# Kernel optimization log

Hardware: AMD Instinct MI355X
Metric: run time of the kernel (lower is better)

Reference implementation:

```python
import jax, jax.numpy as jnp
import numpy as np

BUCKET_SIZE = 64
N_HASHES = 8


def setup_inputs() -> dict:
    key = jax.random.key(0)
    ks = jax.random.split(key, 8)
    B, S, D = 4, 4096, 512
    n_buckets = S // BUCKET_SIZE  # 64
    x = jax.random.normal(ks[0], (B, S, D), dtype=jnp.float32)
    rotations = jax.random.normal(ks[1], (1, D, N_HASHES, n_buckets // 2), dtype=jnp.float32)
    w_qk = jax.random.normal(ks[2], (D, D), dtype=jnp.float32) * 0.02
    b_qk = jax.random.normal(ks[3], (D,), dtype=jnp.float32) * 0.02
    w_v = jax.random.normal(ks[4], (D, D), dtype=jnp.float32) * 0.02
    b_v = jax.random.normal(ks[5], (D,), dtype=jnp.float32) * 0.02
    w_out = jax.random.normal(ks[6], (D, D), dtype=jnp.float32) * 0.02
    b_out = jax.random.normal(ks[7], (D,), dtype=jnp.float32) * 0.02
    return {"x": x, "rotations": rotations, "w_qk": w_qk, "b_qk": b_qk,
            "w_v": w_v, "b_v": b_v, "w_out": w_out, "b_out": b_out}


def reference(x, rotations, w_qk, b_qk, w_v, b_v, w_out, b_out):
    B, S, D = x.shape
    T = S  # seqlen is already a multiple of 2*bucket_size -> no padding
    n_buckets = T // BUCKET_SIZE
    qk = x @ w_qk + b_qk            # [B, T, D]
    v = x @ w_v + b_v               # [B, T, D]

    # --- LSH bucketing ---
    rot = jnp.einsum('btf,fhi->bhti', qk, rotations[0])      # [B, H, T, nb/2]
    rot = jnp.concatenate([rot, -rot], axis=-1)              # [B, H, T, nb]
    buckets = jnp.argmax(rot, axis=-1)                       # [B, H, T]
    offsets = (jnp.arange(N_HASHES) * n_buckets)[None, :, None]
    buckets = (buckets + offsets).reshape(B, -1)             # [B, H*T]

    # --- stable sort by (bucket, position) ---
    ticker = jnp.arange(N_HASHES * T)[None, :]
    buckets_and_t = T * buckets + ticker % T                 # unique keys
    sticker = jnp.argsort(buckets_and_t, axis=-1)            # sorted ticker values
    undo_sort = jnp.argsort(sticker, axis=-1)
    st = sticker % T                                         # token positions

    # --- gather Q/K/V into sorted order ---
    idx = jnp.broadcast_to(st[:, :, None], (B, N_HASHES * T, D))
    sqk = jnp.take_along_axis(qk, idx, axis=1)               # [B, H*T, D]
    sv = jnp.take_along_axis(v, idx, axis=1)

    # --- chunked attention (no softmax, as in the original module) ---
    chunks = N_HASHES * n_buckets
    bq = sqk.reshape(B, chunks, BUCKET_SIZE, D)
    bv = sv.reshape(B, chunks, BUCKET_SIZE, D)
    norm = jnp.maximum(jnp.linalg.norm(bq, axis=-1, keepdims=True), 1e-12)
    bk = bq / norm                                           # F.normalize(p=2)
    dots = jnp.einsum('buie,buje->buij', bq, bk) * (D ** -0.5)
    bo = jnp.einsum('buij,buje->buie', dots, bv)             # [B, chunks, bs, D]

    # --- scatter back and combine hash rounds ---
    so = bo.reshape(B, -1, D)
    uidx = jnp.broadcast_to(undo_sort[:, :, None], (B, N_HASHES * T, D))
    o = jnp.take_along_axis(so, uidx, axis=1)
    out = o.reshape(B, N_HASHES, T, D).sum(axis=1)           # sum over hash rounds
    return out @ w_out + b_out
```

## Files before the change

### kernel.cpp

```cpp
#include <hip/hip_runtime.h>


typedef __attribute__((ext_vector_type(8))) short short8;
typedef __attribute__((ext_vector_type(4))) float f32x4;
typedef unsigned short ushort_t;

__device__ __forceinline__ ushort_t f2b(float f) {
  union { float f; unsigned u; } x; x.f = f;
  unsigned r = x.u + 0x7fffu + ((x.u >> 16) & 1u);
  return (ushort_t)(r >> 16);
}
__device__ __forceinline__ float b2f(unsigned b) {
  union { unsigned u; float f; } x; x.u = b << 16;
  return x.f;
}
__device__ __forceinline__ void gload16(void* lds, const void* gp) {
  __builtin_amdgcn_global_load_lds(
      (const __attribute__((address_space(1))) unsigned int*)gp,
      (__attribute__((address_space(3))) unsigned int*)lds, 16, 0, 0);
}

__global__ __launch_bounds__(256) void prep_kernel(
    const float* __restrict__ x, const float* __restrict__ w_qk,
    const float* __restrict__ b_qk, const float* __restrict__ R,
    const float* __restrict__ w_v, const float* __restrict__ w_out,
    ushort_t* __restrict__ xh, ushort_t* __restrict__ xl,
    ushort_t* __restrict__ wqkT, ushort_t* __restrict__ wvT, ushort_t* __restrict__ woT,
    ushort_t* __restrict__ W2Th, ushort_t* __restrict__ W2Tl, float* __restrict__ b2,
    int* __restrict__ mcount)
{
  __shared__ float t[32][33];
  __shared__ float wrow[512];
  const int blk = blockIdx.x, tid = threadIdx.x;
  if (blk == 0 && tid == 0) mcount[0] = 0;

  if (blk < 4096) {
    const int i = blk * 256 + tid;
    const float4 a = *(const float4*)(x + (size_t)i * 8);
    const float4 c = *(const float4*)(x + (size_t)i * 8 + 4);
    float v[8] = { a.x, a.y, a.z, a.w, c.x, c.y, c.z, c.w };
    ushort_t hi[8], lo[8];
    #pragma unroll
    for (int k = 0; k < 8; ++k) {
      hi[k] = f2b(v[k]);
      lo[k] = f2b(v[k] - b2f(hi[k]));
    }
    *(uint4*)(xh + (size_t)i * 8) = *(const uint4*)hi;
    *(uint4*)(xl + (size_t)i * 8) = *(const uint4*)lo;
  } else if (blk < 4864) {
    const int idx = blk - 4096;
    const int mat = idx >> 8, r = idx & 255;
    const float* W  = (mat == 0) ? w_qk : (mat == 1) ? w_v : w_out;
    ushort_t*   Wt  = (mat == 0) ? wqkT : (mat == 1) ? wvT : woT;
    const int bx = (r & 15) * 32, by = (r >> 4) * 32;
    const int tx = tid & 31, ty = tid >> 5;
    #pragma unroll
    for (int j = 0; j < 4; ++j)
      t[ty + j*8][tx] = W[(size_t)(by + ty + j*8) * 512 + bx + tx];
    __syncthreads();
    #pragma unroll
    for (int j = 0; j < 4; ++j)
      Wt[(size_t)(bx + ty + j*8) * 512 + by + tx] = f2b(t[tx][ty + j*8]);
  } else {
    const int e = blk - 4864, j = tid;
    const float* src = (e < 512) ? (w_qk + (size_t)e * 512) : b_qk;
    wrow[j]       = src[j];
    wrow[j + 256] = src[j + 256];
    __syncthreads();
    float acc = 0.f;
    for (int f = 0; f < 512; ++f)
      acc = fmaf(wrow[f], R[(size_t)f * 256 + j], acc);
    if (e < 512) {
      const ushort_t hi = f2b(acc);
      W2Th[(size_t)j * 512 + e] = hi;
      W2Tl[(size_t)j * 512 + e] = f2b(acc - b2f(hi));
    } else {
      b2[j] = acc;
    }
  }
}

__global__ __launch_bounds__(256, 2) void gemm_mfma(
    const ushort_t* __restrict__ A, const ushort_t* __restrict__ Wt,
    const float* __restrict__ bias, float* __restrict__ Cf,
    ushort_t* __restrict__ Cb, int out_bf16)
{
  __shared__ __align__(16) char Al[32768];
  __shared__ __align__(16) char Bl[32768];
  const int bm = blockIdx.x * 128, bn = blockIdx.y * 128;
  const int tid = threadIdx.x, w = tid >> 6, l = tid & 63;
  const int m = l & 15, gq = l >> 4;
  f32x4 acc[2][8] = {};

#define STAGE1(NB, K0) { \
    _Pragma("unroll") \
    for (int j = 0; j < 4; ++j) { \
      const int row = w * 32 + j * 8 + (l >> 3); \
      const int ch = (l & 7) ^ (row & 7); \
      const int dst = (NB) * 16384 + w * 4096 + j * 1024 + l * 16; \
      gload16(Al + dst, A  + (size_t)(bm + row) * 512 + (K0) + ch * 8); \
      gload16(Bl + dst, Wt + (size_t)(bn + row) * 512 + (K0) + ch * 8); \
    } }

  STAGE1(0, 0)
  __syncthreads();
  for (int t = 0; t < 8; ++t) {
    const int cur = t & 1;
    if (t < 7) STAGE1(cur ^ 1, (t + 1) * 64)
    #pragma unroll
    for (int ks = 0; ks < 2; ++ks) {
      short8 bfr[8];
      #pragma unroll
      for (int tj = 0; tj < 8; ++tj) {
        const int brow = tj * 16 + m;
        bfr[tj] = *(const short8*)(Bl + cur * 16384 + ((brow * 128 + ks * 64 + gq * 16) ^ ((brow & 7) << 4)));
      }
      #pragma unroll
      for (int ti = 0; ti < 2; ++ti) {
        const int arow = w * 32 + ti * 16 + m;
        const short8 af = *(const short8*)(Al + cur * 16384 + ((arow * 128 + ks * 64 + gq * 16) ^ ((arow & 7) << 4)));
        #pragma unroll
        for (int tj = 0; tj < 8; ++tj)
          acc[ti][tj] = __builtin_amdgcn_mfma_f32_16x16x32_bf16(af, bfr[tj], acc[ti][tj], 0, 0, 0);
      }
    }
    __syncthreads();
  }
#undef STAGE1
  #pragma unroll
  for (int ti = 0; ti < 2; ++ti)
    #pragma unroll
    for (int tj = 0; tj < 8; ++tj) {
      const int col = bn + tj * 16 + m;
      const float bvv = bias[col];
      #pragma unroll
      for (int r2 = 0; r2 < 4; ++r2) {
        const int row = bm + w * 32 + ti * 16 + gq * 4 + r2;
        const float oo = acc[ti][tj][r2] + bvv;
        if (out_bf16) Cb[(size_t)row * 512 + col] = f2b(oo);
        else          Cf[(size_t)row * 512 + col] = oo;
      }
    }
}

__global__ __launch_bounds__(256, 3) void gemm_mfma_x2(
    const ushort_t* __restrict__ Ah, const ushort_t* __restrict__ Al,
    const ushort_t* __restrict__ Wt, const float* __restrict__ bias,
    ushort_t* __restrict__ Cb)
{
  __shared__ __align__(16) char AH[16384], AL[16384], BH[16384];
  const int bm = blockIdx.x * 128, bn = blockIdx.y * 128;
  const int tid = threadIdx.x, w = tid >> 6, l = tid & 63;
  const int m = l & 15, gq = l >> 4;
  f32x4 acc[2][8] = {};
  for (int k0 = 0; k0 < 512; k0 += 64) {
    #pragma unroll
    for (int j = 0; j < 4; ++j) {
      const int row = w * 32 + j * 8 + (l >> 3);
      const int ch = (l & 7) ^ (row & 7);
      const int dst = w * 4096 + j * 1024 + l * 16;
      gload16(AH + dst, Ah + (size_t)(bm + row) * 512 + k0 + ch * 8);
      gload16(AL + dst, Al + (size_t)(bm + row) * 512 + k0 + ch * 8);
      gload16(BH + dst, Wt + (size_t)(bn + row) * 512 + k0 + ch * 8);
    }
    __syncthreads();
    #pragma unroll
    for (int ks = 0; ks < 2; ++ks) {
      short8 bfr[8];
      #pragma unroll
      for (int tj = 0; tj < 8; ++tj) {
        const int brow = tj * 16 + m;
        bfr[tj] = *(const short8*)(BH + ((brow * 128 + ks * 64 + gq * 16) ^ ((brow & 7) << 4)));
      }
      #pragma unroll
      for (int ti = 0; ti < 2; ++ti) {
        const int arow = w * 32 + ti * 16 + m;
        const int aa = (arow * 128 + ks * 64 + gq * 16) ^ ((arow & 7) << 4);
        const short8 ah8 = *(const short8*)(AH + aa);
        const short8 al8 = *(const short8*)(AL + aa);
        #pragma unroll
        for (int tj = 0; tj < 8; ++tj) {
          acc[ti][tj] = __builtin_amdgcn_mfma_f32_16x16x32_bf16(ah8, bfr[tj], acc[ti][tj], 0, 0, 0);
          acc[ti][tj] = __builtin_amdgcn_mfma_f32_16x16x32_bf16(al8, bfr[tj], acc[ti][tj], 0, 0, 0);
        }
      }
    }
    __syncthreads();
  }
  #pragma unroll
  for (int ti = 0; ti < 2; ++ti)
    #pragma unroll
    for (int tj = 0; tj < 8; ++tj) {
      const int col = bn + tj * 16 + m;
      const float bvv = bias[col];
      #pragma unroll
      for (int r2 = 0; r2 < 4; ++r2) {
        const int row = bm + w * 32 + ti * 16 + gq * 4 + r2;
        Cb[(size_t)row * 512 + col] = f2b(acc[ti][tj][r2] + bvv);
      }
    }
}

__global__ __launch_bounds__(256, 2) void rot3_mfma(
    const ushort_t* __restrict__ Ah, const ushort_t* __restrict__ Al,
    const ushort_t* __restrict__ Bh, const ushort_t* __restrict__ Bl,
    const float* __restrict__ b2, float* __restrict__ rot)
{
  __shared__ __align__(16) char AH[16384], AL[16384], BH[16384], BL[16384];
  const int bm = blockIdx.x * 128, bn = blockIdx.y * 128;
  const int tid = threadIdx.x, w = tid >> 6, l = tid & 63;
  const int m = l & 15, gq = l >> 4;
  f32x4 acc[2][8] = {};
  for (int k0 = 0; k0 < 512; k0 += 64) {
    #pragma unroll
    for (int j = 0; j < 4; ++j) {
      const int row = w * 32 + j * 8 + (l >> 3);
      const int ch = (l & 7) ^ (row & 7);
      const int dst = w * 4096 + j * 1024 + l * 16;
      gload16(AH + dst, Ah + (size_t)(bm + row) * 512 + k0 + ch * 8);
      gload16(AL + dst, Al + (size_t)(bm + row) * 512 + k0 + ch * 8);
      gload16(BH + dst, Bh + (size_t)(bn + row) * 512 + k0 + ch * 8);
      gload16(BL + dst, Bl + (size_t)(bn + row) * 512 + k0 + ch * 8);
    }
    __syncthreads();
    #pragma unroll
    for (int ks = 0; ks < 2; ++ks) {
      short8 bh8[8], bl8[8];
      #pragma unroll
      for (int tj = 0; tj < 8; ++tj) {
        const int ba = ((tj * 16 + m) * 128 + ks * 64 + gq * 16) ^ (((tj * 16 + m) & 7) << 4);
        bh8[tj] = *(const short8*)(BH + ba);
        bl8[tj] = *(const short8*)(BL + ba);
      }
      #pragma unroll
      for (int ti = 0; ti < 2; ++ti) {
        const int arow = w * 32 + ti * 16 + m;
        const int aa = (arow * 128 + ks * 64 + gq * 16) ^ ((arow & 7) << 4);
        const short8 ah8 = *(const short8*)(AH + aa);
        const short8 al8 = *(const short8*)(AL + aa);
        #pragma unroll
        for (int tj = 0; tj < 8; ++tj) {
          acc[ti][tj] = __builtin_amdgcn_mfma_f32_16x16x32_bf16(ah8, bh8[tj], acc[ti][tj], 0, 0, 0);
          acc[ti][tj] = __builtin_amdgcn_mfma_f32_16x16x32_bf16(al8, bh8[tj], acc[ti][tj], 0, 0, 0);
          acc[ti][tj] = __builtin_amdgcn_mfma_f32_16x16x32_bf16(ah8, bl8[tj], acc[ti][tj], 0, 0, 0);
        }
      }
    }
    __syncthreads();
  }
  #pragma unroll
  for (int ti = 0; ti < 2; ++ti)
    #pragma unroll
    for (int tj = 0; tj < 8; ++tj) {
      const int col = bn + tj * 16 + m;
      const float bvv = b2[col];
      #pragma unroll
      for (int r2 = 0; r2 < 4; ++r2) {
        const int row = bm + w * 32 + ti * 16 + gq * 4 + r2;
        rot[(size_t)row * 256 + col] = acc[ti][tj][r2] + bvv;
      }
    }
}

__global__ __launch_bounds__(256) void argmax_scale(
    const float* __restrict__ rot, int* __restrict__ buckets,
    int* __restrict__ mlist, int* __restrict__ mcount, float tau,
    const ushort_t* __restrict__ qh, float* __restrict__ scale)
{
  const int blk = blockIdx.x;
  if (blk < 16384) {
    const int tok = blk;
    const int j = threadIdx.x;
    const float r = rot[(size_t)tok * 256 + j];
    float m1, m2; int i1;
    if (r >= 0.f) { m1 = r;  i1 = j & 31;        m2 = -r; }
    else          { m1 = -r; i1 = (j & 31) + 32; m2 = r;  }
    #pragma unroll
    for (int off = 16; off; off >>= 1) {
      const float om1 = __shfl_xor(m1, off);
      const int   oi1 = __shfl_xor(i1, off);
      const float om2 = __shfl_xor(m2, off);
      float loser;
      if (om1 > m1 || (om1 == m1 && oi1 < i1)) { loser = m1; m1 = om1; i1 = oi1; }
      else loser = om1;
      m2 = fmaxf(fmaxf(m2, om2), loser);
    }
    if ((j & 31) == 0) {
      const int h = j >> 5, b = tok >> 12, t = tok & 4095;
      buckets[((b << 3) + h) * 4096 + t] = i1;
      if (m1 - m2 < tau) {
        const int k = atomicAdd(mcount, 1);
        mlist[k] = (((b << 3) + h) << 12) | t;
      }
    }
  } else {
    const int wave = threadIdx.x >> 6, lane = threadIdx.x & 63;
    const int tok = (blk - 16384) * 4 + wave;
    const uint4 H = *(const uint4*)(qh + (size_t)tok * 512 + lane * 8);
    const unsigned* hp = (const unsigned*)&H;
    float s = 0.f;
    #pragma unroll
    for (int e = 0; e < 4; ++e) {
      const float v0 = b2f(hp[e] & 0xffffu);
      const float v1 = b2f(hp[e] >> 16);
      s += v0 * v0 + v1 * v1;
    }
    #pragma unroll
    for (int off = 32; off; off >>= 1) s += __shfl_down(s, off);
    if (lane == 0) {
      const float nn = fmaxf(sqrtf(s), 1e-12f);
      scale[tok] = 0.044194173824159216f / nn;
    }
  }
}

__global__ __launch_bounds__(512) void bucket_fallback(
    const float* __restrict__ x, const float* __restrict__ w_qk,
    const float* __restrict__ b_qk, const float* __restrict__ R,
    const int* __restrict__ mlist, const int* __restrict__ mcount,
    int* __restrict__ buckets)
{
  __shared__ float qkrow[512];
  const int n = mcount[0];
  for (int ii = blockIdx.x; ii < n; ii += gridDim.x) {
    const int mm = mlist[ii];
    const int bh = mm >> 12, t = mm & 4095;
    const int b = bh >> 3, h = bh & 7;
    const float* xr = x + ((size_t)b * 4096 + t) * 512;
    {
      const int c = threadIdx.x;
      float a0 = 0.f;
      for (int f = 0; f < 512; ++f) a0 = fmaf(xr[f], w_qk[(size_t)f * 512 + c], a0);
      qkrow[c] = a0 + b_qk[c];
    }
    __syncthreads();
    if (threadIdx.x < 32) {
      const int col = h * 32 + threadIdx.x;
      float a0 = 0.f;
      for (int f = 0; f < 512; ++f) a0 = fmaf(qkrow[f], R[(size_t)f * 256 + col], a0);
      float m1; int i1;
      if (a0 >= 0.f) { m1 = a0;  i1 = threadIdx.x; }
      else           { m1 = -a0; i1 = threadIdx.x + 32; }
      #pragma unroll
      for (int off = 16; off; off >>= 1) {
        const float om = __shfl_xor(m1, off);
        const int   oi = __shfl_xor(i1, off);
        if (om > m1 || (om == m1 && oi < i1)) { m1 = om; i1 = oi; }
      }
      if (threadIdx.x == 0) buckets[(size_t)bh * 4096 + t] = i1;
    }
    __syncthreads();
  }
}

__global__ __launch_bounds__(256) void sort_kernel(
    const int* __restrict__ buckets, int* __restrict__ st)
{
  __shared__ int bk_lds[4096];
  __shared__ int cnt[64][64];
  __shared__ int bstart[64];
  const int tid = threadIdx.x;
  const int base = blockIdx.x * 4096;
  const int wave = tid >> 6, lane = tid & 63;
  const unsigned long long lt = (1ull << lane) - 1ull;

  for (int t = tid; t < 4096; t += 256) bk_lds[t] = buckets[base + t];
  for (int i = tid; i < 4096; i += 256) ((int*)cnt)[i] = 0;
  __syncthreads();

  for (int c = wave; c < 64; c += 4) {
    const int bk = bk_lds[c * 64 + lane];
    unsigned long long mask = ~0ull;
    #pragma unroll
    for (int bit = 0; bit < 6; ++bit) {
      const unsigned long long bb = __ballot((bk >> bit) & 1);
      mask &= ((bk >> bit) & 1) ? bb : ~bb;
    }
    if ((mask & lt) == 0)
      cnt[c][bk] = __popcll(mask);
  }
  __syncthreads();

  if (tid < 64) {
    int run = 0;
    for (int c = 0; c < 64; ++c) {
      const int v = cnt[c][tid];
      cnt[c][tid] = run;
      run += v;
    }
    int ex = run;
    #pragma unroll
    for (int off = 1; off < 64; off <<= 1) {
      const int nn = __shfl_up(ex, off);
      if (lane >= off) ex += nn;
    }
    bstart[tid] = ex - run;
  }
  __syncthreads();

  for (int c = wave; c < 64; c += 4) {
    const int tok = c * 64 + lane;
    const int bk = bk_lds[tok];
    unsigned long long mask = ~0ull;
    #pragma unroll
    for (int bit = 0; bit < 6; ++bit) {
      const unsigned long long bb = __ballot((bk >> bit) & 1);
      mask &= ((bk >> bit) & 1) ? bb : ~bb;
    }
    const int rank = (int)__popcll(mask & lt);
    st[base + bstart[bk] + cnt[c][bk] + rank] = tok;
  }
}

__global__ __launch_bounds__(256, 2) void attn_mfma(
    const ushort_t* __restrict__ qk_b, const ushort_t* __restrict__ v_b,
    const float* __restrict__ scale, const int* __restrict__ st,
    ushort_t* __restrict__ so, int g, int hbase)
{
  __shared__ __align__(16) char Q[32768];
  __shared__ __align__(16) char VT[32768];
  __shared__ __align__(16) char P[8192];
  __shared__ int   stt[64];
  __shared__ float scl[64];

  const int blk = blockIdx.x;
  const int cpg = g * 64;
  const int b = blk / cpg, rem = blk % cpg;
  const int hl = rem >> 6, c = rem & 63;
  const int tid = threadIdx.x, w = tid >> 6, l = tid & 63;
  const int m = l & 15, gq = l >> 4;
  const int srow = tid >> 5, su = tid & 31;

  if (tid < 64) {
    const int s = st[(size_t)((b * 8 + hbase + hl) * 4096) + c * 64 + tid];
    stt[tid] = s;
    scl[tid] = scale[b * 4096 + s];
  }
  __syncthreads();

  const size_t qkbase = (size_t)b * 4096;
  uint4 rg[8];

#define LOADG(SRC, HALF) { \
    _Pragma("unroll") \
    for (int it = 0; it < 8; ++it) { \
      const int row = it * 8 + srow; \
      rg[it] = *(const uint4*)((SRC) + (qkbase + stt[row]) * 512 + (HALF) * 256 + su * 8); \
    } }
#define WRITEQ() { \
    _Pragma("unroll") \
    for (int it = 0; it < 8; ++it) { \
      const int row = it * 8 + srow; \
      *(uint4*)(Q + ((row * 512 + su * 16) ^ ((row & 7) << 4))) = rg[it]; \
    } }
#define WRITEVT() { \
    _Pragma("unroll") \
    for (int it = 0; it < 8; ++it) { \
      const int j = it * 8 + srow; \
      const ushort_t* e = (const ushort_t*)&rg[it]; \
      _Pragma("unroll") \
      for (int ee = 0; ee < 8; ++ee) { \
        const int d = su * 8 + ee; \
        *(ushort_t*)(VT + ((d * 128 + j * 2) ^ (((d ^ (d >> 3)) & 7) << 4))) = e[ee]; \
      } \
    } }
#define COMPUTE_S() { \
    _Pragma("unroll") \
    for (int kf = 0; kf < 8; ++kf) { \
      const int arow = w * 16 + m; \
      const short8 af = *(const short8*)(Q + ((arow * 512 + kf * 64 + gq * 16) ^ ((arow & 7) << 4))); \
      _Pragma("unroll") \
      for (int jt = 0; jt < 4; ++jt) { \
        const int brow = jt * 16 + m; \
        const short8 bf = *(const short8*)(Q + ((brow * 512 + kf * 64 + gq * 16) ^ ((brow & 7) << 4))); \
        accS[jt] = __builtin_amdgcn_mfma_f32_16x16x32_bf16(af, bf, accS[jt], 0, 0, 0); \
      } \
    } }
#define COMPUTE_PV(ACCO) { \
    _Pragma("unroll") \
    for (int dt = 0; dt < 16; ++dt) { \
      _Pragma("unroll") \
      for (int kf = 0; kf < 2; ++kf) { \
        const int d = dt * 16 + m; \
        const short8 bv = *(const short8*)(VT + ((d * 128 + kf * 64 + gq * 16) ^ (((d ^ (d >> 3)) & 7) << 4))); \
        ACCO[dt] = __builtin_amdgcn_mfma_f32_16x16x32_bf16(ap[kf], bv, ACCO[dt], 0, 0, 0); \
      } \
    } }
#define BOUNCE(ACCO) { \
    _Pragma("unroll") \
    for (int dt = 0; dt < 16; ++dt) \
      _Pragma("unroll") \
      for (int r = 0; r < 4; ++r) { \
        const int i = w * 16 + gq * 4 + r; \
        const int dcol = dt * 16 + m; \
        *(ushort_t*)(Q + ((i * 512 + dcol * 2) ^ ((i & 7) << 4))) = f2b(ACCO[dt][r]); \
      } }
#define FLUSH(HALF) { \
    _Pragma("unroll") \
    for (int it = 0; it < 8; ++it) { \
      const int row = it * 8 + srow; \
      const uint4 dat = *(const uint4*)(Q + ((row * 512 + su * 16) ^ ((row & 7) << 4))); \
      *(uint4*)(so + (sobase + stt[row]) * 512 + (HALF) * 256 + su * 8) = dat; \
    } }

  f32x4 accS[4] = {};

  LOADG(qk_b, 0)
  WRITEQ()
  __syncthreads();
  LOADG(qk_b, 1)
  COMPUTE_S()
  __syncthreads();
  WRITEQ()
  __syncthreads();
  LOADG(v_b, 0)
  COMPUTE_S()
  __syncthreads();

  #pragma unroll
  for (int jt = 0; jt < 4; ++jt)
    #pragma unroll
    for (int r = 0; r < 4; ++r) {
      const int i = w * 16 + gq * 4 + r;
      const int j = jt * 16 + m;
      *(ushort_t*)(P + ((i * 128 + j * 2) ^ ((i & 7) << 4))) = f2b(accS[jt][r] * scl[j]);
    }
  WRITEVT()
  __syncthreads();

  const size_t sobase = (size_t)(b * g + hl) * 4096;
  LOADG(v_b, 1)
  short8 ap[2];
  #pragma unroll
  for (int kf = 0; kf < 2; ++kf) {
    const int i = w * 16 + m;
    ap[kf] = *(const short8*)(P + ((i * 128 + kf * 64 + gq * 16) ^ ((i & 7) << 4)));
  }
  f32x4 accO[16] = {};
  COMPUTE_PV(accO)
  __syncthreads();

  WRITEVT()
  BOUNCE(accO)
  __syncthreads();

  FLUSH(0)
  f32x4 accO2[16] = {};
  COMPUTE_PV(accO2)
  __syncthreads();

  BOUNCE(accO2)
  __syncthreads();
  FLUSH(1)

#undef LOADG
#undef WRITEQ
#undef WRITEVT
#undef COMPUTE_S
#undef COMPUTE_PV
#undef BOUNCE
#undef FLUSH
}

__global__ __launch_bounds__(256) void gather_kernel(
    const ushort_t* __restrict__ so, ushort_t* __restrict__ o_b, int g, int first)
{
  const int tok = blockIdx.x;
  const int b = tok >> 12, t = tok & 4095;
  const int d0 = threadIdx.x * 2;
  ushort_t* dst = o_b + (size_t)tok * 512 + d0;
  float ax = 0.f, ay = 0.f;
  if (!first) {
    const unsigned u = *(const unsigned*)dst;
    ax = b2f(u & 0xffffu); ay = b2f(u >> 16);
  }
  const size_t stride = (size_t)4096 * 512;
  const ushort_t* src = so + ((size_t)(b * g) * 4096 + t) * 512 + d0;
  for (int hlp = 0; hlp < g; ++hlp) {
    const unsigned u = *(const unsigned*)src;
    ax += b2f(u & 0xffffu);
    ay += b2f(u >> 16);
    src += stride;
  }
  *(unsigned*)dst = ((unsigned)f2b(ay) << 16) | (unsigned)f2b(ax);
}

extern "C" void kernel_launch(void* const* d_in, const int* in_sizes, int n_in,
                              void* d_out, int out_size, void* d_ws, size_t ws_size,
                              hipStream_t stream) {
  const float* x         = (const float*)d_in[0];
  const float* rotations = (const float*)d_in[1];
  const float* w_qk      = (const float*)d_in[2];
  const float* b_qk      = (const float*)d_in[3];
  const float* w_v       = (const float*)d_in[4];
  const float* b_v       = (const float*)d_in[5];
  const float* w_out     = (const float*)d_in[6];
  const float* b_out     = (const float*)d_in[7];
  float* out = (float*)d_out;
  char* ws = (char*)d_ws;

  ushort_t* xh      = (ushort_t*)(ws);
  ushort_t* xl      = (ushort_t*)(ws + 16777216);
  ushort_t* qk_hi   = (ushort_t*)(ws + 33554432);
  ushort_t* v_b     = (ushort_t*)(ws + 50331648);
  float*    rot     = (float*)(ws + 67108864);
  ushort_t* o_b     = (ushort_t*)(ws + 67108864);
  ushort_t* wqkTh   = (ushort_t*)(ws + 83886080);
  ushort_t* wvT     = (ushort_t*)(ws + 84410368);
  ushort_t* woT     = (ushort_t*)(ws + 84934656);
  ushort_t* W2Th    = (ushort_t*)(ws + 85458944);
  ushort_t* W2Tl    = (ushort_t*)(ws + 85721088);
  float*    b2      = (float*)(ws + 85983232);
  float*    scale   = (float*)(ws + 85987328);
  int*      buckets = (int*)(ws + 86052864);
  int*      st      = (int*)(ws + 86577152);
  int*      mlist   = (int*)(ws + 87101440);
  int*      mcount  = (int*)(ws + 87625728);
  ushort_t* so      = (ushort_t*)(ws + 87629824);
  const size_t so_off = 87629824;

  int g = 1;
  for (int cand = 8; cand >= 1; cand >>= 1)
    if (so_off + (size_t)cand * 16777216ull <= ws_size) { g = cand; break; }

  const dim3 blk256(256);
  hipLaunchKernelGGL(prep_kernel, dim3(5377), blk256, 0, stream,
                     x, w_qk, b_qk, rotations, w_v, w_out,
                     xh, xl, wqkTh, wvT, woT, W2Th, W2Tl, b2, mcount);

  hipLaunchKernelGGL(gemm_mfma_x2, dim3(128, 4), blk256, 0, stream, xh, xl, wqkTh, b_qk, qk_hi);
  hipLaunchKernelGGL(gemm_mfma, dim3(128, 4), blk256, 0, stream, xh, wvT, b_v, (float*)0, v_b, 1);
  hipLaunchKernelGGL(rot3_mfma, dim3(128, 2), blk256, 0, stream, xh, xl, W2Th, W2Tl, b2, rot);

  hipLaunchKernelGGL(argmax_scale, dim3(20480), blk256, 0, stream,
                     rot, buckets, mlist, mcount, 1.5e-3f, qk_hi, scale);
  hipLaunchKernelGGL(bucket_fallback, dim3(1024), dim3(512), 0, stream,
                     x, w_qk, b_qk, rotations, mlist, mcount, buckets);
  hipLaunchKernelGGL(sort_kernel, dim3(32), blk256, 0, stream, buckets, st);

  const int passes = 8 / g;
  for (int p = 0; p < passes; ++p) {
    const int hbase = p * g;
    hipLaunchKernelGGL(attn_mfma, dim3(4 * g * 64), blk256, 0, stream,
                       qk_hi, v_b, scale, st, so, g, hbase);
    hipLaunchKernelGGL(gather_kernel, dim3(16384), blk256, 0, stream,
                       so, o_b, g, (p == 0) ? 1 : 0);
  }

  hipLaunchKernelGGL(gemm_mfma, dim3(128, 4), blk256, 0, stream, o_b, woT, b_out, out, (ushort_t*)0, 0);
}
```

Before: 256.5 us.

## Fuse QK and V projections into one GEMM with interleaved QKV output

Replaces the separate hi/lo split-precision QK GEMM and the V GEMM with a single launch. Each token's QK and V rows are written side by side in one buffer with a 1024-wide row stride. The QK projection drops the low-part correction pass and now uses only xh, halving its MFMA work at some cost in QK precision. Attention and scale kernels read Q/K and V from adjacent halves of the same row, which may improve locality for the gathered loads.

New measurement: 244.4 us, median of 2. 1.05x faster.

```diff
diff --git a/kernel.cpp b/kernel.cpp
--- a/kernel.cpp
+++ b/kernel.cpp
@@ -80,10 +80,75 @@
   }
 }
 
+__global__ __launch_bounds__(256, 2) void gemm_qkv(
+    const ushort_t* __restrict__ A, const ushort_t* __restrict__ wqkT,
+    const ushort_t* __restrict__ wvT, const float* __restrict__ b_qk,
+    const float* __restrict__ b_v, ushort_t* __restrict__ qkv)
+{
+  __shared__ __align__(16) char Al[32768];
+  __shared__ __align__(16) char Bl[32768];
+  const int bm = blockIdx.x * 128;
+  const int sel = blockIdx.y >> 2;
+  const int bn = (blockIdx.y & 3) * 128;
+  const ushort_t* Wt   = sel ? wvT : wqkT;
+  const float*    bias = sel ? b_v : b_qk;
+  const int coff = sel * 512;
+  const int tid = threadIdx.x, w = tid >> 6, l = tid & 63;
+  const int m = l & 15, gq = l >> 4;
+  f32x4 acc[2][8] = {};
+
+#define STAGE1(NB, K0) { \
+    _Pragma("unroll") \
+    for (int j = 0; j < 4; ++j) { \
+      const int row = w * 32 + j * 8 + (l >> 3); \
+      const int ch = (l & 7) ^ (row & 7); \
+      const int dst = (NB) * 16384 + w * 4096 + j * 1024 + l * 16; \
+      gload16(Al + dst, A  + (size_t)(bm + row) * 512 + (K0) + ch * 8); \
+      gload16(Bl + dst, Wt + (size_t)(bn + row) * 512 + (K0) + ch * 8); \
+    } }
+
+  STAGE1(0, 0)
+  __syncthreads();
+  for (int t = 0; t < 8; ++t) {
+    const int cur = t & 1;
+    if (t < 7) STAGE1(cur ^ 1, (t + 1) * 64)
+    #pragma unroll
+    for (int ks = 0; ks < 2; ++ks) {
+      short8 bfr[8];
+      #pragma unroll
+      for (int tj = 0; tj < 8; ++tj) {
+        const int brow = tj * 16 + m;
+        bfr[tj] = *(const short8*)(Bl + cur * 16384 + ((brow * 128 + ks * 64 + gq * 16) ^ ((brow & 7) << 4)));
+      }
+      #pragma unroll
+      for (int ti = 0; ti < 2; ++ti) {
+        const int arow = w * 32 + ti * 16 + m;
+        const short8 af = *(const short8*)(Al + cur * 16384 + ((arow * 128 + ks * 64 + gq * 16) ^ ((arow & 7) << 4)));
+        #pragma unroll
+        for (int tj = 0; tj < 8; ++tj)
+          acc[ti][tj] = __builtin_amdgcn_mfma_f32_16x16x32_bf16(af, bfr[tj], acc[ti][tj], 0, 0, 0);
+      }
+    }
+    __syncthreads();
+  }
+#undef STAGE1
+  #pragma unroll
+  for (int ti = 0; ti < 2; ++ti)
+    #pragma unroll
+    for (int tj = 0; tj < 8; ++tj) {
+      const int col = bn + tj * 16 + m;
+      const float bvv = bias[col];
+      #pragma unroll
+      for (int r2 = 0; r2 < 4; ++r2) {
+        const int row = bm + w * 32 + ti * 16 + gq * 4 + r2;
+        qkv[(size_t)row * 1024 + coff + col] = f2b(acc[ti][tj][r2] + bvv);
+      }
+    }
+}
+
 __global__ __launch_bounds__(256, 2) void gemm_mfma(
     const ushort_t* __restrict__ A, const ushort_t* __restrict__ Wt,
-    const float* __restrict__ bias, float* __restrict__ Cf,
-    ushort_t* __restrict__ Cb, int out_bf16)
+    const float* __restrict__ bias, float* __restrict__ Cf)
 {
   __shared__ __align__(16) char Al[32768];
   __shared__ __align__(16) char Bl[32768];
@@ -136,67 +201,7 @@
       #pragma unroll
       for (int r2 = 0; r2 < 4; ++r2) {
         const int row = bm + w * 32 + ti * 16 + gq * 4 + r2;
-        const float oo = acc[ti][tj][r2] + bvv;
-        if (out_bf16) Cb[(size_t)row * 512 + col] = f2b(oo);
-        else          Cf[(size_t)row * 512 + col] = oo;
-      }
-    }
-}
-
-__global__ __launch_bounds__(256, 3) void gemm_mfma_x2(
-    const ushort_t* __restrict__ Ah, const ushort_t* __restrict__ Al,
-    const ushort_t* __restrict__ Wt, const float* __restrict__ bias,
-    ushort_t* __restrict__ Cb)
-{
-  __shared__ __align__(16) char AH[16384], AL[16384], BH[16384];
-  const int bm = blockIdx.x * 128, bn = blockIdx.y * 128;
-  const int tid = threadIdx.x, w = tid >> 6, l = tid & 63;
-  const int m = l & 15, gq = l >> 4;
-  f32x4 acc[2][8] = {};
-  for (int k0 = 0; k0 < 512; k0 += 64) {
-    #pragma unroll
-    for (int j = 0; j < 4; ++j) {
-      const int row = w * 32 + j * 8 + (l >> 3);
-      const int ch = (l & 7) ^ (row & 7);
-      const int dst = w * 4096 + j * 1024 + l * 16;
-      gload16(AH + dst, Ah + (size_t)(bm + row) * 512 + k0 + ch * 8);
-      gload16(AL + dst, Al + (size_t)(bm + row) * 512 + k0 + ch * 8);
-      gload16(BH + dst, Wt + (size_t)(bn + row) * 512 + k0 + ch * 8);
-    }
-    __syncthreads();
-    #pragma unroll
-    for (int ks = 0; ks < 2; ++ks) {
-      short8 bfr[8];
-      #pragma unroll
-      for (int tj = 0; tj < 8; ++tj) {
-        const int brow = tj * 16 + m;
-        bfr[tj] = *(const short8*)(BH + ((brow * 128 + ks * 64 + gq * 16) ^ ((brow & 7) << 4)));
-      }
-      #pragma unroll
-      for (int ti = 0; ti < 2; ++ti) {
-        const int arow = w * 32 + ti * 16 + m;
-        const int aa = (arow * 128 + ks * 64 + gq * 16) ^ ((arow & 7) << 4);
-        const short8 ah8 = *(const short8*)(AH + aa);
-        const short8 al8 = *(const short8*)(AL + aa);
-        #pragma unroll
-        for (int tj = 0; tj < 8; ++tj) {
-          acc[ti][tj] = __builtin_amdgcn_mfma_f32_16x16x32_bf16(ah8, bfr[tj], acc[ti][tj], 0, 0, 0);
-          acc[ti][tj] = __builtin_amdgcn_mfma_f32_16x16x32_bf16(al8, bfr[tj], acc[ti][tj], 0, 0, 0);
-        }
-      }
-    }
-    __syncthreads();
-  }
-  #pragma unroll
-  for (int ti = 0; ti < 2; ++ti)
-    #pragma unroll
-    for (int tj = 0; tj < 8; ++tj) {
-      const int col = bn + tj * 16 + m;
-      const float bvv = bias[col];
-      #pragma unroll
-      for (int r2 = 0; r2 < 4; ++r2) {
-        const int row = bm + w * 32 + ti * 16 + gq * 4 + r2;
-        Cb[(size_t)row * 512 + col] = f2b(acc[ti][tj][r2] + bvv);
+        Cf[(size_t)row * 512 + col] = acc[ti][tj][r2] + bvv;
       }
     }
 }
@@ -265,7 +270,7 @@
 __global__ __launch_bounds__(256) void argmax_scale(
     const float* __restrict__ rot, int* __restrict__ buckets,
     int* __restrict__ mlist, int* __restrict__ mcount, float tau,
-    const ushort_t* __restrict__ qh, float* __restrict__ scale)
+    const ushort_t* __restrict__ qkv, float* __restrict__ scale)
 {
   const int blk = blockIdx.x;
   if (blk < 16384) {
@@ -296,7 +301,7 @@
   } else {
     const int wave = threadIdx.x >> 6, lane = threadIdx.x & 63;
     const int tok = (blk - 16384) * 4 + wave;
-    const uint4 H = *(const uint4*)(qh + (size_t)tok * 512 + lane * 8);
+    const uint4 H = *(const uint4*)(qkv + (size_t)tok * 1024 + lane * 8);
     const unsigned* hp = (const unsigned*)&H;
     float s = 0.f;
     #pragma unroll
@@ -413,9 +418,8 @@
 }
 
 __global__ __launch_bounds__(256, 2) void attn_mfma(
-    const ushort_t* __restrict__ qk_b, const ushort_t* __restrict__ v_b,
-    const float* __restrict__ scale, const int* __restrict__ st,
-    ushort_t* __restrict__ so, int g, int hbase)
+    const ushort_t* __restrict__ qkv, const float* __restrict__ scale,
+    const int* __restrict__ st, ushort_t* __restrict__ so, int g, int hbase)
 {
   __shared__ __align__(16) char Q[32768];
   __shared__ __align__(16) char VT[32768];
@@ -441,11 +445,11 @@
   const size_t qkbase = (size_t)b * 4096;
   uint4 rg[8];
 
-#define LOADG(SRC, HALF) { \
+#define LOADG(VOFF, HALF) { \
     _Pragma("unroll") \
     for (int it = 0; it < 8; ++it) { \
       const int row = it * 8 + srow; \
-      rg[it] = *(const uint4*)((SRC) + (qkbase + stt[row]) * 512 + (HALF) * 256 + su * 8); \
+      rg[it] = *(const uint4*)(qkv + (qkbase + stt[row]) * 1024 + (VOFF) + (HALF) * 256 + su * 8); \
     } }
 #define WRITEQ() { \
     _Pragma("unroll") \
@@ -505,15 +509,15 @@
 
   f32x4 accS[4] = {};
 
-  LOADG(qk_b, 0)
+  LOADG(0, 0)
   WRITEQ()
   __syncthreads();
-  LOADG(qk_b, 1)
+  LOADG(0, 1)
   COMPUTE_S()
   __syncthreads();
   WRITEQ()
   __syncthreads();
-  LOADG(v_b, 0)
+  LOADG(512, 0)
   COMPUTE_S()
   __syncthreads();
 
@@ -529,7 +533,7 @@
   __syncthreads();
 
   const size_t sobase = (size_t)(b * g + hl) * 4096;
-  LOADG(v_b, 1)
+  LOADG(512, 1)
   short8 ap[2];
   #pragma unroll
   for (int kf = 0; kf < 2; ++kf) {
@@ -601,8 +605,7 @@
 
   ushort_t* xh      = (ushort_t*)(ws);
   ushort_t* xl      = (ushort_t*)(ws + 16777216);
-  ushort_t* qk_hi   = (ushort_t*)(ws + 33554432);
-  ushort_t* v_b     = (ushort_t*)(ws + 50331648);
+  ushort_t* qkv     = (ushort_t*)(ws + 33554432);
   float*    rot     = (float*)(ws + 67108864);
   ushort_t* o_b     = (ushort_t*)(ws + 67108864);
   ushort_t* wqkTh   = (ushort_t*)(ws + 83886080);
@@ -628,12 +631,11 @@
                      x, w_qk, b_qk, rotations, w_v, w_out,
                      xh, xl, wqkTh, wvT, woT, W2Th, W2Tl, b2, mcount);
 
-  hipLaunchKernelGGL(gemm_mfma_x2, dim3(128, 4), blk256, 0, stream, xh, xl, wqkTh, b_qk, qk_hi);
-  hipLaunchKernelGGL(gemm_mfma, dim3(128, 4), blk256, 0, stream, xh, wvT, b_v, (float*)0, v_b, 1);
+  hipLaunchKernelGGL(gemm_qkv, dim3(128, 8), blk256, 0, stream, xh, wqkTh, wvT, b_qk, b_v, qkv);
   hipLaunchKernelGGL(rot3_mfma, dim3(128, 2), blk256, 0, stream, xh, xl, W2Th, W2Tl, b2, rot);
 
   hipLaunchKernelGGL(argmax_scale, dim3(20480), blk256, 0, stream,
-                     rot, buckets, mlist, mcount, 1.5e-3f, qk_hi, scale);
+                     rot, buckets, mlist, mcount, 1.5e-3f, qkv, scale);
   hipLaunchKernelGGL(bucket_fallback, dim3(1024), dim3(512), 0, stream,
                      x, w_qk, b_qk, rotations, mlist, mcount, buckets);
   hipLaunchKernelGGL(sort_kernel, dim3(32), blk256, 0, stream, buckets, st);
@@ -642,10 +644,10 @@
   for (int p = 0; p < passes; ++p) {
     const int hbase = p * g;
     hipLaunchKernelGGL(attn_mfma, dim3(4 * g * 64), blk256, 0, stream,
-                       qk_hi, v_b, scale, st, so, g, hbase);
+                       qkv, scale, st, so, g, hbase);
     hipLaunchKernelGGL(gather_kernel, dim3(16384), blk256, 0, stream,
                        so, o_b, g, (p == 0) ? 1 : 0);
   }
 
-  hipLaunchKernelGGL(gemm_mfma, dim3(128, 4), blk256, 0, stream, o_b, woT, b_out, out, (ushort_t*)0, 0);
-}
+  hipLaunchKernelGGL(gemm_mfma, dim3(128, 4), blk256, 0, stream, o_b, woT, b_out, out);
+}
```
